# Optimization experiments

Hardware: AMD Instinct MI355X
Metric: run time of the kernel (lower is better)

Reference implementation:

```python
import jax, jax.numpy as jnp
import numpy as np

N_NODES = 50000
N_EDGES = 1600000
IN_C = 64
OUT_C = 64
N_CLASSES = 45


def setup_inputs() -> dict:
    key = jax.random.key(0)
    ks = jax.random.split(key, 12)

    def lin(k, i, o):
        return jax.random.normal(k, (i, o), jnp.float32) / np.float32(np.sqrt(i))

    return dict(
        x=jax.random.normal(ks[0], (N_NODES, IN_C), jnp.float32),
        edge_index=jax.random.randint(ks[1], (2, N_EDGES), 0, N_NODES, dtype=jnp.int32),
        W_z=lin(ks[2], IN_C, OUT_C), b_z=jnp.zeros((OUT_C,), jnp.float32),
        Wl_z=lin(ks[3], 2 * OUT_C, OUT_C), bl_z=jnp.zeros((OUT_C,), jnp.float32),
        W_r=lin(ks[4], IN_C, OUT_C), b_r=jnp.zeros((OUT_C,), jnp.float32),
        Wl_r=lin(ks[5], 2 * OUT_C, OUT_C), bl_r=jnp.zeros((OUT_C,), jnp.float32),
        W_h=lin(ks[6], IN_C, OUT_C), b_h=jnp.zeros((OUT_C,), jnp.float32),
        Wl_h=lin(ks[7], 2 * OUT_C, OUT_C), bl_h=jnp.zeros((OUT_C,), jnp.float32),
        W_out=lin(ks[8], OUT_C, N_CLASSES), b_out=jnp.zeros((N_CLASSES,), jnp.float32),
    )


def _gcn(x, W, b, src, dst, dinv):
    # GCNConv with improved self-loops (fill value 2.0):
    # out = D^{-1/2} (A + 2I) D^{-1/2} X W + b, with deg = in_degree + 2
    xw = x @ W                                   # [N, OUT_C]
    norm = dinv[src] * dinv[dst]                 # [E]
    agg = jax.ops.segment_sum(norm[:, None] * xw[src], dst, num_segments=N_NODES)
    agg = agg + (2.0 * dinv * dinv)[:, None] * xw  # self-loop contribution
    return agg + b


def reference(x, edge_index, W_z, b_z, Wl_z, bl_z, W_r, b_r, Wl_r, bl_r,
              W_h, b_h, Wl_h, bl_h, W_out, b_out):
    src, dst = edge_index[0], edge_index[1]
    deg = jax.ops.segment_sum(jnp.ones((N_EDGES,), jnp.float32), dst,
                              num_segments=N_NODES) + 2.0
    dinv = jax.lax.rsqrt(deg)

    # TGCN cell with H0 = 0 (no prior hidden state passed)
    H = jnp.zeros((N_NODES, OUT_C), x.dtype)
    Z = jax.nn.sigmoid(
        jnp.concatenate([_gcn(x, W_z, b_z, src, dst, dinv), H], axis=1) @ Wl_z + bl_z)
    R = jax.nn.sigmoid(
        jnp.concatenate([_gcn(x, W_r, b_r, src, dst, dinv), H], axis=1) @ Wl_r + bl_r)
    H_tilde = jnp.tanh(
        jnp.concatenate([_gcn(x, W_h, b_h, src, dst, dinv), H * R], axis=1) @ Wl_h + bl_h)
    H = Z * H + (1.0 - Z) * H_tilde

    # relu + linear readout to 45 classes
    return jax.nn.relu(H) @ W_out + b_out
```

## Files before the change

### kernel.cpp

```cpp
#include <hip/hip_runtime.h>

#define N_NODES 50000
#define N_EDGES 1600000
#define NB 782
#define NBB 256
#define CHUNK 6250
#define ZROW 50000
#define NTILES 3125

typedef unsigned short ushort_t;
typedef _Float16 v8h __attribute__((ext_vector_type(8)));
typedef float f32x4_t __attribute__((ext_vector_type(4)));

__device__ __forceinline__ int rlanei(int v, int l) {
  return __builtin_amdgcn_readlane(v, l);
}

__global__ void k_hist(const int* __restrict__ ei, int* __restrict__ cnt) {
  __shared__ int h[NB];
  int tid = threadIdx.x, blk = blockIdx.x;
  for (int i = tid; i < NB; i += 256) h[i] = 0;
  __syncthreads();
  int base = blk * CHUNK;
  for (int i = base + tid; i < base + CHUNK; i += 256)
    atomicAdd(&h[ei[N_EDGES + i] >> 6], 1);
  __syncthreads();
  for (int b = tid; b < NB; b += 256) cnt[b * NBB + blk] = h[b];
}

__global__ void k_scanA(const int* __restrict__ cnt, int* __restrict__ bsum) {
  __shared__ int sm[256];
  int t = threadIdx.x;
  sm[t] = cnt[blockIdx.x * 256 + t];
  __syncthreads();
  for (int off = 128; off > 0; off >>= 1) {
    if (t < off) sm[t] += sm[t + off];
    __syncthreads();
  }
  if (t == 0) bsum[blockIdx.x] = sm[0];
}

__global__ void k_scanB(const int* __restrict__ bsum, int* __restrict__ boff) {
  __shared__ int sm[1024];
  int t = threadIdx.x;
  int v = (t < NB) ? bsum[t] : 0;
  sm[t] = v;
  __syncthreads();
  for (int off = 1; off < 1024; off <<= 1) {
    int u = (t >= off) ? sm[t - off] : 0;
    __syncthreads();
    sm[t] += u;
    __syncthreads();
  }
  if (t < NB) boff[t] = sm[t] - v;
  if (t == 0) boff[NB] = N_EDGES;
}

__global__ void k_scanC(int* __restrict__ cnt, const int* __restrict__ boff) {
  __shared__ int sm[256];
  int t = threadIdx.x, j = blockIdx.x;
  int v = cnt[j * 256 + t];
  sm[t] = v;
  __syncthreads();
  for (int off = 1; off < 256; off <<= 1) {
    int u = (t >= off) ? sm[t - off] : 0;
    __syncthreads();
    sm[t] += u;
    __syncthreads();
  }
  cnt[j * 256 + t] = boff[j] + sm[t] - v;
}

__global__ void k_bin(const int* __restrict__ ei, const int* __restrict__ offs,
                      int* __restrict__ bins) {
  __shared__ int cur[NB];
  int tid = threadIdx.x, blk = blockIdx.x;
  for (int b = tid; b < NB; b += 256) cur[b] = offs[b * NBB + blk];
  __syncthreads();
  int base = blk * CHUNK;
  for (int i = base + tid; i < base + CHUNK; i += 256) {
    int s = ei[i];
    int d = ei[N_EDGES + i];
    int b = d >> 6;
    int p = atomicAdd(&cur[b], 1);
    bins[p] = s | ((d & 63) << 16);
  }
}

__global__ __launch_bounds__(256, 4) void k_sort(
    const int* __restrict__ bins, const int* __restrict__ boff,
    const float* __restrict__ x,
    ushort_t* __restrict__ srcp, int2* __restrict__ rowiv,
    float* __restrict__ dinv, _Float16* __restrict__ xp) {
  __shared__ int dg[64], lo[64], cur[64];
  __shared__ float sdin[64];
  __shared__ int Tsh;
  __shared__ ushort_t buf[8192];
  int tid = threadIdx.x, b = blockIdx.x;
  int start = boff[b], end = boff[b + 1];
  if (tid < 64) dg[tid] = 0;
  __syncthreads();
  for (int i = start + tid; i < end; i += 256)
    atomicAdd(&dg[bins[i] >> 16], 1);
  __syncthreads();
  int pdv = 0;
  if (tid < 64) { pdv = (dg[tid] + 7) & ~7; lo[tid] = pdv; }
  __syncthreads();
  for (int off = 1; off < 64; off <<= 1) {
    int u = 0;
    if (tid < 64 && tid >= off) u = lo[tid - off];
    __syncthreads();
    if (tid < 64) lo[tid] += u;
    __syncthreads();
  }
  int ex = 0;
  if (tid < 64) {
    ex = lo[tid] - pdv;
    cur[tid] = ex;
    if (tid == 63) Tsh = lo[63];
  }
  __syncthreads();
  int T = Tsh;
  int base = start + b * 512;
  for (int i = tid; i < T; i += 256) buf[i] = (ushort_t)ZROW;
  __syncthreads();
  for (int i = start + tid; i < end; i += 256) {
    int v = bins[i];
    int dl = v >> 16;
    int p = atomicAdd(&cur[dl], 1);
    buf[p] = (ushort_t)(v & 0xFFFF);
  }
  __syncthreads();
  for (int i = tid; i < T; i += 256) srcp[base + i] = buf[i];
  if (tid < 64) {
    int v = b * 64 + tid;
    if (v < N_NODES) {
      rowiv[v] = make_int2(base + ex, pdv);
      float dv = rsqrtf((float)dg[tid] + 2.0f);
      dinv[v] = dv;
      sdin[tid] = dv;
    } else {
      sdin[tid] = 0.f;
    }
  }
  __syncthreads();
  int nb64 = b * 4096;
  for (int idx = tid; idx < 4096; idx += 256) {
    int v = b * 64 + (idx >> 6);
    if (v < N_NODES) xp[nb64 + idx] = (_Float16)(sdin[idx >> 6] * x[nb64 + idx]);
  }
  if (b == 0 && tid < 64) xp[ZROW * 64 + tid] = (_Float16)0.f;
}

__global__ void k_compose(const float* __restrict__ Wz, const float* __restrict__ bz,
                          const float* __restrict__ Wlz, const float* __restrict__ blz,
                          const float* __restrict__ Wh, const float* __restrict__ bh,
                          const float* __restrict__ Wlh, const float* __restrict__ blh,
                          float2* __restrict__ M, float2* __restrict__ B2) {
  int t = blockIdx.x * 256 + threadIdx.x;
  if (t < 4096) {
    int i = t >> 6, c = t & 63;
    float mz = 0.f, mh = 0.f;
    for (int j = 0; j < 64; ++j) {
      mz = fmaf(Wz[i * 64 + j], Wlz[j * 64 + c], mz);
      mh = fmaf(Wh[i * 64 + j], Wlh[j * 64 + c], mh);
    }
    M[t] = make_float2(mz, mh);
  } else if (t < 4160) {
    int c = t - 4096;
    float vz = blz[c], vh = blh[c];
    for (int j = 0; j < 64; ++j) {
      vz = fmaf(bz[j], Wlz[j * 64 + c], vz);
      vh = fmaf(bh[j], Wlh[j * 64 + c], vh);
    }
    B2[c] = make_float2(vz, vh);
  }
}

__global__ void k_pack(const float2* __restrict__ M, const float* __restrict__ Wout,
                       _Float16* __restrict__ Bzh, _Float16* __restrict__ Bwo) {
  int t = blockIdx.x * 256 + threadIdx.x;
  if (t < 8192) {
    int frag = t >> 9, lane = (t >> 3) & 63, j = t & 7;
    int ntile = frag >> 1, ks = frag & 1;
    int n = ntile * 16 + (lane & 15);
    int k = ks * 32 + ((lane >> 4) << 3) + j;
    float v = (n < 64) ? M[k * 64 + n].x : M[k * 64 + (n - 64)].y;
    Bzh[t] = (_Float16)v;
  } else if (t < 11264) {
    int u = t - 8192;
    int frag = u >> 9, lane = (u >> 3) & 63, j = u & 7;
    int ntile = frag >> 1, ks = frag & 1;
    int n = ntile * 16 + (lane & 15);
    int k = ks * 32 + ((lane >> 4) << 3) + j;
    Bwo[u] = (_Float16)((n < 45) ? Wout[k * 45 + n] : 0.f);
  }
}

__global__ __launch_bounds__(256) void k_agg(
    const ushort_t* __restrict__ srcp, const int2* __restrict__ rowiv,
    const float* __restrict__ dinv, const _Float16* __restrict__ xp,
    _Float16* __restrict__ sxg) {
  int tid = threadIdx.x;
  int lane = tid & 63;
  int w = blockIdx.x * 4 + (tid >> 6);
  int nw = gridDim.x * 4;
  for (int v = w; v < N_NODES; v += nw) {
    int vu = __builtin_amdgcn_readfirstlane(v);
    int2 ri = rowiv[vu];
    int beg = ri.x, pd = ri.y;
    float a0 = 0.f, a1 = 0.f;
    for (int e = beg; e < beg + pd; e += 64) {
      int rem = beg + pd - e;
      int m = rem < 64 ? rem : 64;
      int sv = ZROW;
      if (lane < m) sv = srcp[e + lane];
      for (int j = 0; j < m; j += 8) {
        int s0 = rlanei(sv, j),     s1 = rlanei(sv, j + 1);
        int s2 = rlanei(sv, j + 2), s3 = rlanei(sv, j + 3);
        int s4 = rlanei(sv, j + 4), s5 = rlanei(sv, j + 5);
        int s6 = rlanei(sv, j + 6), s7 = rlanei(sv, j + 7);
        a0 += (float)xp[s0 * 64 + lane];
        a1 += (float)xp[s1 * 64 + lane];
        a0 += (float)xp[s2 * 64 + lane];
        a1 += (float)xp[s3 * 64 + lane];
        a0 += (float)xp[s4 * 64 + lane];
        a1 += (float)xp[s5 * 64 + lane];
        a0 += (float)xp[s6 * 64 + lane];
        a1 += (float)xp[s7 * 64 + lane];
      }
    }
    float dv = dinv[vu];
    float self = (float)xp[vu * 64 + lane];
    sxg[vu * 64 + lane] = (_Float16)(dv * (a0 + a1) + 2.f * dv * self);
  }
}

__global__ __launch_bounds__(256) void k_cell(
    const _Float16* __restrict__ sxg, const _Float16* __restrict__ Bzh,
    const _Float16* __restrict__ Bwo, const float2* __restrict__ B2,
    const float* __restrict__ bout, float* __restrict__ out) {
  __shared__ __align__(16) _Float16 tbuf[4][16][72];
  int tid = threadIdx.x;
  int lane = tid & 63, wv = tid >> 6;
  int l15 = lane & 15, quad = lane >> 4;
  int tile = blockIdx.x * 4 + wv;
  if (tile >= NTILES) return;

  v8h bz[8][2], bw[3][2];
  #pragma unroll
  for (int t = 0; t < 8; ++t)
    #pragma unroll
    for (int ks = 0; ks < 2; ++ks)
      bz[t][ks] = *(const v8h*)(Bzh + (((t * 2 + ks) * 64 + lane) << 3));
  #pragma unroll
  for (int t = 0; t < 3; ++t)
    #pragma unroll
    for (int ks = 0; ks < 2; ++ks)
      bw[t][ks] = *(const v8h*)(Bwo + (((t * 2 + ks) * 64 + lane) << 3));
  float zb[4], hb[4], ob[3];
  #pragma unroll
  for (int t = 0; t < 4; ++t) {
    float2 bb = B2[t * 16 + l15];
    zb[t] = bb.x; hb[t] = bb.y;
  }
  #pragma unroll
  for (int t = 0; t < 3; ++t) {
    int c = t * 16 + l15;
    ob[t] = (c < 45) ? bout[c] : 0.f;
  }

  const _Float16* ar = sxg + (tile * 16 + l15) * 64 + quad * 8;
  v8h a0 = *(const v8h*)ar;
  v8h a1 = *(const v8h*)(ar + 32);

  f32x4_t accz[8];
  #pragma unroll
  for (int t = 0; t < 8; ++t) {
    f32x4_t c4 = {0.f, 0.f, 0.f, 0.f};
    c4 = __builtin_amdgcn_mfma_f32_16x16x32_f16(a0, bz[t][0], c4, 0, 0, 0);
    c4 = __builtin_amdgcn_mfma_f32_16x16x32_f16(a1, bz[t][1], c4, 0, 0, 0);
    accz[t] = c4;
  }

  #pragma unroll
  for (int t = 0; t < 4; ++t) {
    #pragma unroll
    for (int r = 0; r < 4; ++r) {
      float zv = accz[t][r] + zb[t];
      float hv = accz[t + 4][r] + hb[t];
      float Z = 1.f / (1.f + __expf(-zv));
      float tt = fminf(15.f, fmaxf(-15.f, hv));
      float e2 = __expf(-2.f * tt);
      float Th = (1.f - e2) / (1.f + e2);
      tbuf[wv][quad * 4 + r][t * 16 + l15] = (_Float16)fmaxf((1.f - Z) * Th, 0.f);
    }
  }
  __asm__ volatile("s_waitcnt lgkmcnt(0)" ::: "memory");

  v8h p0 = *(const v8h*)&tbuf[wv][l15][quad * 8];
  v8h p1 = *(const v8h*)&tbuf[wv][l15][32 + quad * 8];

  #pragma unroll
  for (int t = 0; t < 3; ++t) {
    f32x4_t o4 = {0.f, 0.f, 0.f, 0.f};
    o4 = __builtin_amdgcn_mfma_f32_16x16x32_f16(p0, bw[t][0], o4, 0, 0, 0);
    o4 = __builtin_amdgcn_mfma_f32_16x16x32_f16(p1, bw[t][1], o4, 0, 0, 0);
    int c = t * 16 + l15;
    if (c < 45) {
      #pragma unroll
      for (int r = 0; r < 4; ++r)
        out[(tile * 16 + quad * 4 + r) * 45 + c] = o4[r] + ob[t];
    }
  }
}

extern "C" void kernel_launch(void* const* d_in, const int* in_sizes, int n_in,
                              void* d_out, int out_size, void* d_ws, size_t ws_size,
                              hipStream_t stream) {
  const float* x    = (const float*)d_in[0];
  const int*   ei   = (const int*)d_in[1];
  const float* Wz   = (const float*)d_in[2];
  const float* bz   = (const float*)d_in[3];
  const float* Wlz  = (const float*)d_in[4];
  const float* blz  = (const float*)d_in[5];
  const float* Wh   = (const float*)d_in[10];
  const float* bh   = (const float*)d_in[11];
  const float* Wlh  = (const float*)d_in[12];
  const float* blh  = (const float*)d_in[13];
  const float* Wout = (const float*)d_in[14];
  const float* bout = (const float*)d_in[15];
  float* out = (float*)d_out;

  char* w = (char*)d_ws;
  int*      cnt   = (int*)(w + 0);
  int*      bins  = (int*)(w + 800768);
  _Float16* sxg   = (_Float16*)(w + 0);
  ushort_t* srcp  = (ushort_t*)(w + 12800000);
  int2*     rowiv = (int2*)(w + 16801024);
  float*    dinv  = (float*)(w + 17201024);
  int*      bsum  = (int*)(w + 17401024);
  int*      boff  = (int*)(w + 17404160);
  float2*   M     = (float2*)(w + 17407360);
  float2*   B2    = (float2*)(w + 17440128);
  _Float16* Bzh   = (_Float16*)(w + 17440768);
  _Float16* Bwo   = (_Float16*)(w + 17457152);
  _Float16* xp    = (_Float16*)(w + 17463296);

  k_hist <<<NBB, 256, 0, stream>>>(ei, cnt);
  k_scanA<<<NB, 256, 0, stream>>>(cnt, bsum);
  k_scanB<<<1, 1024, 0, stream>>>(bsum, boff);
  k_scanC<<<NB, 256, 0, stream>>>(cnt, boff);
  k_bin  <<<NBB, 256, 0, stream>>>(ei, cnt, bins);
  k_sort <<<NB, 256, 0, stream>>>(bins, boff, x, srcp, rowiv, dinv, xp);
  k_compose<<<17, 256, 0, stream>>>(Wz, bz, Wlz, blz, Wh, bh, Wlh, blh, M, B2);
  k_pack <<<44, 256, 0, stream>>>(M, Wout, Bzh, Bwo);
  k_agg  <<<2048, 256, 0, stream>>>(srcp, rowiv, dinv, xp, sxg);
  k_cell <<<NB, 256, 0, stream>>>(sxg, Bzh, Bwo, B2, bout, out);
}
```

Measured before the change: 191.8 us.

## Fuse CSR build into one cooperative kernel with grid syncs; merge weight prep

Replaces the histogram, three scan kernels, binning and per-bucket sort kernels with a single cooperative kernel that uses grid.sync between phases. Each block bins its edge chunk locally in shared memory and records per-bucket local offsets, then gathers its bucket's edges from every chunk. The weight composition and packing kernels are merged into one kernel that writes MFMA-layout fragments directly. The aim is to cut kernel launch count and inter-kernel gaps, at the cost of grid-wide barriers, a scattered gather of many tiny segments per block, and a requirement that all 782 blocks be co-resident.

```diff
diff --git a/kernel.cpp b/kernel.cpp
--- a/kernel.cpp
+++ b/kernel.cpp
@@ -1,10 +1,12 @@
 #include <hip/hip_runtime.h>
+#include <hip/hip_cooperative_groups.h>
+namespace cg = cooperative_groups;
 
 #define N_NODES 50000
 #define N_EDGES 1600000
 #define NB 782
-#define NBB 256
-#define CHUNK 6250
+#define NBK 782
+#define CH 2048
 #define ZROW 50000
 #define NTILES 3125
 
@@ -16,92 +18,116 @@
   return __builtin_amdgcn_readlane(v, l);
 }
 
-__global__ void k_hist(const int* __restrict__ ei, int* __restrict__ cnt) {
+__global__ __launch_bounds__(256, 4) void k_build(
+    const int* __restrict__ ei, int* __restrict__ cnt, int* __restrict__ bsum,
+    ushort_t* __restrict__ loc, int* __restrict__ bins,
+    const float* __restrict__ x, ushort_t* __restrict__ srcp,
+    int2* __restrict__ rowiv, float* __restrict__ dinv,
+    _Float16* __restrict__ xp) {
   __shared__ int h[NB];
+  __shared__ int hB[NB];
+  __shared__ int ebuf[3072];
+  __shared__ ushort_t buf[3584];
+  __shared__ int scanTmp[256];
+  __shared__ int dg[64], lo[64], cur64[64];
+  __shared__ float sdin[64];
+  __shared__ int misc[4];
+  cg::grid_group grid = cg::this_grid();
   int tid = threadIdx.x, blk = blockIdx.x;
+  int e0 = blk * CH;
+  int e1 = min(e0 + CH, N_EDGES);
+  int clen = e1 - e0;
+
   for (int i = tid; i < NB; i += 256) h[i] = 0;
   __syncthreads();
-  int base = blk * CHUNK;
-  for (int i = base + tid; i < base + CHUNK; i += 256)
+  for (int i = e0 + tid; i < e1; i += 256)
     atomicAdd(&h[ei[N_EDGES + i] >> 6], 1);
   __syncthreads();
-  for (int b = tid; b < NB; b += 256) cnt[b * NBB + blk] = h[b];
-}
-
-__global__ void k_scanA(const int* __restrict__ cnt, int* __restrict__ bsum) {
-  __shared__ int sm[256];
-  int t = threadIdx.x;
-  sm[t] = cnt[blockIdx.x * 256 + t];
-  __syncthreads();
-  for (int off = 128; off > 0; off >>= 1) {
-    if (t < off) sm[t] += sm[t + off];
-    __syncthreads();
-  }
-  if (t == 0) bsum[blockIdx.x] = sm[0];
-}
-
-__global__ void k_scanB(const int* __restrict__ bsum, int* __restrict__ boff) {
-  __shared__ int sm[1024];
-  int t = threadIdx.x;
-  int v = (t < NB) ? bsum[t] : 0;
-  sm[t] = v;
-  __syncthreads();
-  for (int off = 1; off < 1024; off <<= 1) {
-    int u = (t >= off) ? sm[t - off] : 0;
-    __syncthreads();
-    sm[t] += u;
-    __syncthreads();
-  }
-  if (t < NB) boff[t] = sm[t] - v;
-  if (t == 0) boff[NB] = N_EDGES;
-}
-
-__global__ void k_scanC(int* __restrict__ cnt, const int* __restrict__ boff) {
-  __shared__ int sm[256];
-  int t = threadIdx.x, j = blockIdx.x;
-  int v = cnt[j * 256 + t];
-  sm[t] = v;
-  __syncthreads();
-  for (int off = 1; off < 256; off <<= 1) {
-    int u = (t >= off) ? sm[t - off] : 0;
-    __syncthreads();
-    sm[t] += u;
-    __syncthreads();
-  }
-  cnt[j * 256 + t] = boff[j] + sm[t] - v;
-}
-
-__global__ void k_bin(const int* __restrict__ ei, const int* __restrict__ offs,
-                      int* __restrict__ bins) {
-  __shared__ int cur[NB];
-  int tid = threadIdx.x, blk = blockIdx.x;
-  for (int b = tid; b < NB; b += 256) cur[b] = offs[b * NBB + blk];
-  __syncthreads();
-  int base = blk * CHUNK;
-  for (int i = base + tid; i < base + CHUNK; i += 256) {
-    int s = ei[i];
-    int d = ei[N_EDGES + i];
-    int b = d >> 6;
-    int p = atomicAdd(&cur[b], 1);
-    bins[p] = s | ((d & 63) << 16);
-  }
-}
-
-__global__ __launch_bounds__(256, 4) void k_sort(
-    const int* __restrict__ bins, const int* __restrict__ boff,
-    const float* __restrict__ x,
-    ushort_t* __restrict__ srcp, int2* __restrict__ rowiv,
-    float* __restrict__ dinv, _Float16* __restrict__ xp) {
-  __shared__ int dg[64], lo[64], cur[64];
-  __shared__ float sdin[64];
-  __shared__ int Tsh;
-  __shared__ ushort_t buf[8192];
-  int tid = threadIdx.x, b = blockIdx.x;
-  int start = boff[b], end = boff[b + 1];
+  for (int b = tid; b < NB; b += 256) cnt[blk * NB + b] = h[b];
+  grid.sync();
+
+  {
+    int part = 0;
+    for (int i = tid; i < NBK; i += 256) part += cnt[i * NB + blk];
+    scanTmp[tid] = part;
+    __syncthreads();
+    for (int off = 128; off > 0; off >>= 1) {
+      if (tid < off) scanTmp[tid] += scanTmp[tid + off];
+      __syncthreads();
+    }
+    if (tid == 0) bsum[blk] = scanTmp[0];
+    __syncthreads();
+  }
+
+  {
+    int vals[4]; int ts = 0;
+    int base4 = tid * 4;
+    #pragma unroll
+    for (int r = 0; r < 4; ++r) {
+      int idx = base4 + r;
+      int v = (idx < NB) ? h[idx] : 0;
+      vals[r] = v; ts += v;
+    }
+    scanTmp[tid] = ts;
+    __syncthreads();
+    for (int off = 1; off < 256; off <<= 1) {
+      int u = (tid >= off) ? scanTmp[tid - off] : 0;
+      __syncthreads();
+      scanTmp[tid] += u;
+      __syncthreads();
+    }
+    int ex = scanTmp[tid] - ts;
+    #pragma unroll
+    for (int r = 0; r < 4; ++r) {
+      int idx = base4 + r;
+      if (idx < NB) {
+        hB[idx] = ex;
+        loc[blk * (NB + 1) + idx] = (ushort_t)ex;
+      }
+      ex += vals[r];
+    }
+    if (tid == 0) loc[blk * (NB + 1) + NB] = (ushort_t)clen;
+    __syncthreads();
+    for (int i = e0 + tid; i < e1; i += 256) {
+      int s = ei[i];
+      int d = ei[N_EDGES + i];
+      int p = atomicAdd(&hB[d >> 6], 1);
+      ebuf[p] = s | ((d & 63) << 16);
+    }
+    __syncthreads();
+    for (int i = tid; i < clen; i += 256) bins[e0 + i] = ebuf[i];
+  }
+  grid.sync();
+
+  int b = blk;
+  {
+    int part = 0;
+    for (int j = tid; j < b; j += 256) part += bsum[j];
+    scanTmp[tid] = part;
+    __syncthreads();
+    for (int off = 128; off > 0; off >>= 1) {
+      if (tid < off) scanTmp[tid] += scanTmp[tid + off];
+      __syncthreads();
+    }
+    if (tid == 0) { misc[1] = scanTmp[0]; misc[0] = 0; }
+    __syncthreads();
+  }
+  int boffb = misc[1];
+  for (int j = tid; j < NBK; j += 256) {
+    int l0 = loc[j * (NB + 1) + b];
+    int l1 = loc[j * (NB + 1) + b + 1];
+    int len = l1 - l0;
+    if (len > 0) {
+      int pos = atomicAdd(&misc[0], len);
+      for (int k2 = 0; k2 < len; ++k2)
+        ebuf[pos + k2] = bins[j * CH + l0 + k2];
+    }
+  }
+  __syncthreads();
+  int nEd = misc[0];
   if (tid < 64) dg[tid] = 0;
   __syncthreads();
-  for (int i = start + tid; i < end; i += 256)
-    atomicAdd(&dg[bins[i] >> 16], 1);
+  for (int i = tid; i < nEd; i += 256) atomicAdd(&dg[ebuf[i] >> 16], 1);
   __syncthreads();
   int pdv = 0;
   if (tid < 64) { pdv = (dg[tid] + 7) & ~7; lo[tid] = pdv; }
@@ -113,29 +139,28 @@
     if (tid < 64) lo[tid] += u;
     __syncthreads();
   }
-  int ex = 0;
+  int ex2 = 0;
   if (tid < 64) {
-    ex = lo[tid] - pdv;
-    cur[tid] = ex;
-    if (tid == 63) Tsh = lo[63];
-  }
-  __syncthreads();
-  int T = Tsh;
-  int base = start + b * 512;
+    ex2 = lo[tid] - pdv;
+    cur64[tid] = ex2;
+    if (tid == 63) misc[2] = lo[63];
+  }
+  __syncthreads();
+  int T = misc[2];
+  int sbase = boffb + b * 512;
   for (int i = tid; i < T; i += 256) buf[i] = (ushort_t)ZROW;
   __syncthreads();
-  for (int i = start + tid; i < end; i += 256) {
-    int v = bins[i];
-    int dl = v >> 16;
-    int p = atomicAdd(&cur[dl], 1);
+  for (int i = tid; i < nEd; i += 256) {
+    int v = ebuf[i];
+    int p = atomicAdd(&cur64[v >> 16], 1);
     buf[p] = (ushort_t)(v & 0xFFFF);
   }
   __syncthreads();
-  for (int i = tid; i < T; i += 256) srcp[base + i] = buf[i];
+  for (int i = tid; i < T; i += 256) srcp[sbase + i] = buf[i];
   if (tid < 64) {
     int v = b * 64 + tid;
     if (v < N_NODES) {
-      rowiv[v] = make_int2(base + ex, pdv);
+      rowiv[v] = make_int2(sbase + ex2, pdv);
       float dv = rsqrtf((float)dg[tid] + 2.0f);
       dinv[v] = dv;
       sdin[tid] = dv;
@@ -152,48 +177,43 @@
   if (b == 0 && tid < 64) xp[ZROW * 64 + tid] = (_Float16)0.f;
 }
 
-__global__ void k_compose(const float* __restrict__ Wz, const float* __restrict__ bz,
-                          const float* __restrict__ Wlz, const float* __restrict__ blz,
-                          const float* __restrict__ Wh, const float* __restrict__ bh,
-                          const float* __restrict__ Wlh, const float* __restrict__ blh,
-                          float2* __restrict__ M, float2* __restrict__ B2) {
+__global__ __launch_bounds__(256) void k_wprep(
+    const float* __restrict__ Wz, const float* __restrict__ bz,
+    const float* __restrict__ Wlz, const float* __restrict__ blz,
+    const float* __restrict__ Wh, const float* __restrict__ bh,
+    const float* __restrict__ Wlh, const float* __restrict__ blh,
+    const float* __restrict__ Wout,
+    float2* __restrict__ B2, _Float16* __restrict__ Bzh,
+    _Float16* __restrict__ Bwo) {
   int t = blockIdx.x * 256 + threadIdx.x;
-  if (t < 4096) {
-    int i = t >> 6, c = t & 63;
-    float mz = 0.f, mh = 0.f;
-    for (int j = 0; j < 64; ++j) {
-      mz = fmaf(Wz[i * 64 + j], Wlz[j * 64 + c], mz);
-      mh = fmaf(Wh[i * 64 + j], Wlh[j * 64 + c], mh);
-    }
-    M[t] = make_float2(mz, mh);
-  } else if (t < 4160) {
-    int c = t - 4096;
-    float vz = blz[c], vh = blh[c];
-    for (int j = 0; j < 64; ++j) {
-      vz = fmaf(bz[j], Wlz[j * 64 + c], vz);
-      vh = fmaf(bh[j], Wlh[j * 64 + c], vh);
-    }
-    B2[c] = make_float2(vz, vh);
-  }
-}
-
-__global__ void k_pack(const float2* __restrict__ M, const float* __restrict__ Wout,
-                       _Float16* __restrict__ Bzh, _Float16* __restrict__ Bwo) {
-  int t = blockIdx.x * 256 + threadIdx.x;
-  if (t < 8192) {
-    int frag = t >> 9, lane = (t >> 3) & 63, j = t & 7;
-    int ntile = frag >> 1, ks = frag & 1;
+  {
+    int lane = (t >> 3) & 63, j = t & 7;
+    int ntile = t >> 10, ks = (t >> 9) & 1;
     int n = ntile * 16 + (lane & 15);
     int k = ks * 32 + ((lane >> 4) << 3) + j;
-    float v = (n < 64) ? M[k * 64 + n].x : M[k * 64 + (n - 64)].y;
-    Bzh[t] = (_Float16)v;
-  } else if (t < 11264) {
-    int u = t - 8192;
-    int frag = u >> 9, lane = (u >> 3) & 63, j = u & 7;
-    int ntile = frag >> 1, ks = frag & 1;
+    float acc = 0.f;
+    if (n < 64) {
+      for (int q = 0; q < 64; ++q) acc = fmaf(Wz[k * 64 + q], Wlz[q * 64 + n], acc);
+    } else {
+      int n2 = n - 64;
+      for (int q = 0; q < 64; ++q) acc = fmaf(Wh[k * 64 + q], Wlh[q * 64 + n2], acc);
+    }
+    Bzh[t] = (_Float16)acc;
+  }
+  if (t < 3072) {
+    int lane = (t >> 3) & 63, j = t & 7;
+    int ntile = t >> 10, ks = (t >> 9) & 1;
     int n = ntile * 16 + (lane & 15);
     int k = ks * 32 + ((lane >> 4) << 3) + j;
-    Bwo[u] = (_Float16)((n < 45) ? Wout[k * 45 + n] : 0.f);
+    Bwo[t] = (_Float16)((n < 45) ? Wout[k * 45 + n] : 0.f);
+  }
+  if (t < 64) {
+    float vz = blz[t], vh = blh[t];
+    for (int q = 0; q < 64; ++q) {
+      vz = fmaf(bz[q], Wlz[q * 64 + t], vz);
+      vh = fmaf(bh[q], Wlh[q * 64 + t], vh);
+    }
+    B2[t] = make_float2(vz, vh);
   }
 }
 
@@ -247,17 +267,17 @@
   int tile = blockIdx.x * 4 + wv;
   if (tile >= NTILES) return;
 
-  v8h bz[8][2], bw[3][2];
+  v8h bzf[8][2], bwf[3][2];
   #pragma unroll
   for (int t = 0; t < 8; ++t)
     #pragma unroll
     for (int ks = 0; ks < 2; ++ks)
-      bz[t][ks] = *(const v8h*)(Bzh + (((t * 2 + ks) * 64 + lane) << 3));
+      bzf[t][ks] = *(const v8h*)(Bzh + (((t * 2 + ks) * 64 + lane) << 3));
   #pragma unroll
   for (int t = 0; t < 3; ++t)
     #pragma unroll
     for (int ks = 0; ks < 2; ++ks)
-      bw[t][ks] = *(const v8h*)(Bwo + (((t * 2 + ks) * 64 + lane) << 3));
+      bwf[t][ks] = *(const v8h*)(Bwo + (((t * 2 + ks) * 64 + lane) << 3));
   float zb[4], hb[4], ob[3];
   #pragma unroll
   for (int t = 0; t < 4; ++t) {
@@ -278,8 +298,8 @@
   #pragma unroll
   for (int t = 0; t < 8; ++t) {
     f32x4_t c4 = {0.f, 0.f, 0.f, 0.f};
-    c4 = __builtin_amdgcn_mfma_f32_16x16x32_f16(a0, bz[t][0], c4, 0, 0, 0);
-    c4 = __builtin_amdgcn_mfma_f32_16x16x32_f16(a1, bz[t][1], c4, 0, 0, 0);
+    c4 = __builtin_amdgcn_mfma_f32_16x16x32_f16(a0, bzf[t][0], c4, 0, 0, 0);
+    c4 = __builtin_amdgcn_mfma_f32_16x16x32_f16(a1, bzf[t][1], c4, 0, 0, 0);
     accz[t] = c4;
   }
 
@@ -304,8 +324,8 @@
   #pragma unroll
   for (int t = 0; t < 3; ++t) {
     f32x4_t o4 = {0.f, 0.f, 0.f, 0.f};
-    o4 = __builtin_amdgcn_mfma_f32_16x16x32_f16(p0, bw[t][0], o4, 0, 0, 0);
-    o4 = __builtin_amdgcn_mfma_f32_16x16x32_f16(p1, bw[t][1], o4, 0, 0, 0);
+    o4 = __builtin_amdgcn_mfma_f32_16x16x32_f16(p0, bwf[t][0], o4, 0, 0, 0);
+    o4 = __builtin_amdgcn_mfma_f32_16x16x32_f16(p1, bwf[t][1], o4, 0, 0, 0);
     int c = t * 16 + l15;
     if (c < 45) {
       #pragma unroll
@@ -334,27 +354,27 @@
 
   char* w = (char*)d_ws;
   int*      cnt   = (int*)(w + 0);
-  int*      bins  = (int*)(w + 800768);
+  int*      bins  = (int*)(w + 2446096);
+  ushort_t* loc   = (ushort_t*)(w + 8846096);
+  int*      bsum  = (int*)(w + 10070720);
   _Float16* sxg   = (_Float16*)(w + 0);
-  ushort_t* srcp  = (ushort_t*)(w + 12800000);
-  int2*     rowiv = (int2*)(w + 16801024);
-  float*    dinv  = (float*)(w + 17201024);
-  int*      bsum  = (int*)(w + 17401024);
-  int*      boff  = (int*)(w + 17404160);
-  float2*   M     = (float2*)(w + 17407360);
-  float2*   B2    = (float2*)(w + 17440128);
-  _Float16* Bzh   = (_Float16*)(w + 17440768);
-  _Float16* Bwo   = (_Float16*)(w + 17457152);
-  _Float16* xp    = (_Float16*)(w + 17463296);
-
-  k_hist <<<NBB, 256, 0, stream>>>(ei, cnt);
-  k_scanA<<<NB, 256, 0, stream>>>(cnt, bsum);
-  k_scanB<<<1, 1024, 0, stream>>>(bsum, boff);
-  k_scanC<<<NB, 256, 0, stream>>>(cnt, boff);
-  k_bin  <<<NBB, 256, 0, stream>>>(ei, cnt, bins);
-  k_sort <<<NB, 256, 0, stream>>>(bins, boff, x, srcp, rowiv, dinv, xp);
-  k_compose<<<17, 256, 0, stream>>>(Wz, bz, Wlz, blz, Wh, bh, Wlh, blh, M, B2);
-  k_pack <<<44, 256, 0, stream>>>(M, Wout, Bzh, Bwo);
-  k_agg  <<<2048, 256, 0, stream>>>(srcp, rowiv, dinv, xp, sxg);
-  k_cell <<<NB, 256, 0, stream>>>(sxg, Bzh, Bwo, B2, bout, out);
-}
+  ushort_t* srcp  = (ushort_t*)(w + 10073856);
+  int2*     rowiv = (int2*)(w + 14074624);
+  float*    dinv  = (float*)(w + 14474624);
+  float2*   B2    = (float2*)(w + 14674624);
+  _Float16* Bzh   = (_Float16*)(w + 14675136);
+  _Float16* Bwo   = (_Float16*)(w + 14691520);
+  _Float16* xp    = (_Float16*)(w + 14697664);
+
+  k_wprep<<<32, 256, 0, stream>>>(Wz, bz, Wlz, blz, Wh, bh, Wlh, blh, Wout,
+                                  B2, Bzh, Bwo);
+  {
+    void* args[] = {(void*)&ei, (void*)&cnt, (void*)&bsum, (void*)&loc,
+                    (void*)&bins, (void*)&x, (void*)&srcp, (void*)&rowiv,
+                    (void*)&dinv, (void*)&xp};
+    hipLaunchCooperativeKernel((const void*)k_build, dim3(NBK), dim3(256),
+                               args, 0, stream);
+  }
+  k_agg <<<2048, 256, 0, stream>>>(srcp, rowiv, dinv, xp, sxg);
+  k_cell<<<NB, 256, 0, stream>>>(sxg, Bzh, Bwo, B2, bout, out);
+}
```

Result: slower. 362.5 us (+89.0%).

## Vectorize agg gathers by splitting wave into 4 edge groups; merge weight-prep kernels

Applied to the files above, without the earlier changes.

The aggregation kernel now splits each wave into four 16-lane groups. Each group gathers a different edge's row using 8-byte half4 loads, with two edges per group per step, and the partial sums are reduced across groups with xor shuffles. Previously each edge took one 2-byte-per-lane load across all 64 lanes. Histogram and binning kernels read edge indices as int2 pairs, and the compose and pack weight kernels are fused into one launch that moves ahead of the graph pipeline. This cuts load instruction count and launch overhead, at the cost of extra cross-lane shuffles and fp32 reductions per node.

```diff
diff --git a/kernel.cpp b/kernel.cpp
--- a/kernel.cpp
+++ b/kernel.cpp
@@ -10,6 +10,7 @@
 
 typedef unsigned short ushort_t;
 typedef _Float16 v8h __attribute__((ext_vector_type(8)));
+typedef _Float16 v4h __attribute__((ext_vector_type(4)));
 typedef float f32x4_t __attribute__((ext_vector_type(4)));
 
 __device__ __forceinline__ int rlanei(int v, int l) {
@@ -21,9 +22,12 @@
   int tid = threadIdx.x, blk = blockIdx.x;
   for (int i = tid; i < NB; i += 256) h[i] = 0;
   __syncthreads();
-  int base = blk * CHUNK;
-  for (int i = base + tid; i < base + CHUNK; i += 256)
-    atomicAdd(&h[ei[N_EDGES + i] >> 6], 1);
+  const int2* d2 = (const int2*)(ei + N_EDGES + blk * CHUNK);
+  for (int i = tid; i < CHUNK / 2; i += 256) {
+    int2 d = d2[i];
+    atomicAdd(&h[d.x >> 6], 1);
+    atomicAdd(&h[d.y >> 6], 1);
+  }
   __syncthreads();
   for (int b = tid; b < NB; b += 256) cnt[b * NBB + blk] = h[b];
 }
@@ -77,13 +81,15 @@
   int tid = threadIdx.x, blk = blockIdx.x;
   for (int b = tid; b < NB; b += 256) cur[b] = offs[b * NBB + blk];
   __syncthreads();
-  int base = blk * CHUNK;
-  for (int i = base + tid; i < base + CHUNK; i += 256) {
-    int s = ei[i];
-    int d = ei[N_EDGES + i];
-    int b = d >> 6;
-    int p = atomicAdd(&cur[b], 1);
-    bins[p] = s | ((d & 63) << 16);
+  const int2* s2 = (const int2*)(ei + blk * CHUNK);
+  const int2* d2 = (const int2*)(ei + N_EDGES + blk * CHUNK);
+  for (int i = tid; i < CHUNK / 2; i += 256) {
+    int2 s = s2[i];
+    int2 d = d2[i];
+    int p0 = atomicAdd(&cur[d.x >> 6], 1);
+    bins[p0] = s.x | ((d.x & 63) << 16);
+    int p1 = atomicAdd(&cur[d.y >> 6], 1);
+    bins[p1] = s.y | ((d.y & 63) << 16);
   }
 }
 
@@ -152,48 +158,43 @@
   if (b == 0 && tid < 64) xp[ZROW * 64 + tid] = (_Float16)0.f;
 }
 
-__global__ void k_compose(const float* __restrict__ Wz, const float* __restrict__ bz,
-                          const float* __restrict__ Wlz, const float* __restrict__ blz,
-                          const float* __restrict__ Wh, const float* __restrict__ bh,
-                          const float* __restrict__ Wlh, const float* __restrict__ blh,
-                          float2* __restrict__ M, float2* __restrict__ B2) {
+__global__ __launch_bounds__(256) void k_wprep(
+    const float* __restrict__ Wz, const float* __restrict__ bz,
+    const float* __restrict__ Wlz, const float* __restrict__ blz,
+    const float* __restrict__ Wh, const float* __restrict__ bh,
+    const float* __restrict__ Wlh, const float* __restrict__ blh,
+    const float* __restrict__ Wout,
+    float2* __restrict__ B2, _Float16* __restrict__ Bzh,
+    _Float16* __restrict__ Bwo) {
   int t = blockIdx.x * 256 + threadIdx.x;
-  if (t < 4096) {
-    int i = t >> 6, c = t & 63;
-    float mz = 0.f, mh = 0.f;
-    for (int j = 0; j < 64; ++j) {
-      mz = fmaf(Wz[i * 64 + j], Wlz[j * 64 + c], mz);
-      mh = fmaf(Wh[i * 64 + j], Wlh[j * 64 + c], mh);
-    }
-    M[t] = make_float2(mz, mh);
-  } else if (t < 4160) {
-    int c = t - 4096;
-    float vz = blz[c], vh = blh[c];
-    for (int j = 0; j < 64; ++j) {
-      vz = fmaf(bz[j], Wlz[j * 64 + c], vz);
-      vh = fmaf(bh[j], Wlh[j * 64 + c], vh);
-    }
-    B2[c] = make_float2(vz, vh);
-  }
-}
-
-__global__ void k_pack(const float2* __restrict__ M, const float* __restrict__ Wout,
-                       _Float16* __restrict__ Bzh, _Float16* __restrict__ Bwo) {
-  int t = blockIdx.x * 256 + threadIdx.x;
-  if (t < 8192) {
-    int frag = t >> 9, lane = (t >> 3) & 63, j = t & 7;
-    int ntile = frag >> 1, ks = frag & 1;
+  {
+    int lane = (t >> 3) & 63, j = t & 7;
+    int ntile = t >> 10, ks = (t >> 9) & 1;
     int n = ntile * 16 + (lane & 15);
     int k = ks * 32 + ((lane >> 4) << 3) + j;
-    float v = (n < 64) ? M[k * 64 + n].x : M[k * 64 + (n - 64)].y;
-    Bzh[t] = (_Float16)v;
-  } else if (t < 11264) {
-    int u = t - 8192;
-    int frag = u >> 9, lane = (u >> 3) & 63, j = u & 7;
-    int ntile = frag >> 1, ks = frag & 1;
+    float acc = 0.f;
+    if (n < 64) {
+      for (int q = 0; q < 64; ++q) acc = fmaf(Wz[k * 64 + q], Wlz[q * 64 + n], acc);
+    } else {
+      int n2 = n - 64;
+      for (int q = 0; q < 64; ++q) acc = fmaf(Wh[k * 64 + q], Wlh[q * 64 + n2], acc);
+    }
+    Bzh[t] = (_Float16)acc;
+  }
+  if (t < 3072) {
+    int lane = (t >> 3) & 63, j = t & 7;
+    int ntile = t >> 10, ks = (t >> 9) & 1;
     int n = ntile * 16 + (lane & 15);
     int k = ks * 32 + ((lane >> 4) << 3) + j;
-    Bwo[u] = (_Float16)((n < 45) ? Wout[k * 45 + n] : 0.f);
+    Bwo[t] = (_Float16)((n < 45) ? Wout[k * 45 + n] : 0.f);
+  }
+  if (t < 64) {
+    float vz = blz[t], vh = blh[t];
+    for (int q = 0; q < 64; ++q) {
+      vz = fmaf(bz[q], Wlz[q * 64 + t], vz);
+      vh = fmaf(bh[q], Wlh[q * 64 + t], vh);
+    }
+    B2[t] = make_float2(vz, vh);
   }
 }
 
@@ -203,36 +204,47 @@
     _Float16* __restrict__ sxg) {
   int tid = threadIdx.x;
   int lane = tid & 63;
+  int grp = lane >> 4;
+  int sub = lane & 15;
+  int chOff = sub << 2;
   int w = blockIdx.x * 4 + (tid >> 6);
   int nw = gridDim.x * 4;
   for (int v = w; v < N_NODES; v += nw) {
     int vu = __builtin_amdgcn_readfirstlane(v);
     int2 ri = rowiv[vu];
     int beg = ri.x, pd = ri.y;
-    float a0 = 0.f, a1 = 0.f;
+    float aA0 = 0.f, aA1 = 0.f, aA2 = 0.f, aA3 = 0.f;
+    float aB0 = 0.f, aB1 = 0.f, aB2 = 0.f, aB3 = 0.f;
     for (int e = beg; e < beg + pd; e += 64) {
       int rem = beg + pd - e;
       int m = rem < 64 ? rem : 64;
-      int sv = ZROW;
-      if (lane < m) sv = srcp[e + lane];
-      for (int j = 0; j < m; j += 8) {
-        int s0 = rlanei(sv, j),     s1 = rlanei(sv, j + 1);
-        int s2 = rlanei(sv, j + 2), s3 = rlanei(sv, j + 3);
-        int s4 = rlanei(sv, j + 4), s5 = rlanei(sv, j + 5);
-        int s6 = rlanei(sv, j + 6), s7 = rlanei(sv, j + 7);
-        a0 += (float)xp[s0 * 64 + lane];
-        a1 += (float)xp[s1 * 64 + lane];
-        a0 += (float)xp[s2 * 64 + lane];
-        a1 += (float)xp[s3 * 64 + lane];
-        a0 += (float)xp[s4 * 64 + lane];
-        a1 += (float)xp[s5 * 64 + lane];
-        a0 += (float)xp[s6 * 64 + lane];
-        a1 += (float)xp[s7 * 64 + lane];
+      int sv = (lane < m) ? (int)srcp[e + lane] : ZROW;
+      for (int t = 0; t < m; t += 8) {
+        int sA = __builtin_amdgcn_ds_bpermute((t + grp) << 2, sv);
+        int sB = __builtin_amdgcn_ds_bpermute((t + 4 + grp) << 2, sv);
+        v4h rA = *(const v4h*)(xp + (sA << 6) + chOff);
+        v4h rB = *(const v4h*)(xp + (sB << 6) + chOff);
+        aA0 += (float)rA[0]; aA1 += (float)rA[1];
+        aA2 += (float)rA[2]; aA3 += (float)rA[3];
+        aB0 += (float)rB[0]; aB1 += (float)rB[1];
+        aB2 += (float)rB[2]; aB3 += (float)rB[3];
       }
     }
-    float dv = dinv[vu];
-    float self = (float)xp[vu * 64 + lane];
-    sxg[vu * 64 + lane] = (_Float16)(dv * (a0 + a1) + 2.f * dv * self);
+    float a0 = aA0 + aB0, a1 = aA1 + aB1, a2 = aA2 + aB2, a3 = aA3 + aB3;
+    a0 += __shfl_xor(a0, 16); a1 += __shfl_xor(a1, 16);
+    a2 += __shfl_xor(a2, 16); a3 += __shfl_xor(a3, 16);
+    a0 += __shfl_xor(a0, 32); a1 += __shfl_xor(a1, 32);
+    a2 += __shfl_xor(a2, 32); a3 += __shfl_xor(a3, 32);
+    if (lane < 16) {
+      float dv = dinv[vu];
+      v4h self = *(const v4h*)(xp + (vu << 6) + chOff);
+      v4h o;
+      o[0] = (_Float16)(dv * a0 + 2.f * dv * (float)self[0]);
+      o[1] = (_Float16)(dv * a1 + 2.f * dv * (float)self[1]);
+      o[2] = (_Float16)(dv * a2 + 2.f * dv * (float)self[2]);
+      o[3] = (_Float16)(dv * a3 + 2.f * dv * (float)self[3]);
+      *(v4h*)(sxg + (vu << 6) + chOff) = o;
+    }
   }
 }
 
@@ -247,17 +259,17 @@
   int tile = blockIdx.x * 4 + wv;
   if (tile >= NTILES) return;
 
-  v8h bz[8][2], bw[3][2];
+  v8h bzf[8][2], bwf[3][2];
   #pragma unroll
   for (int t = 0; t < 8; ++t)
     #pragma unroll
     for (int ks = 0; ks < 2; ++ks)
-      bz[t][ks] = *(const v8h*)(Bzh + (((t * 2 + ks) * 64 + lane) << 3));
+      bzf[t][ks] = *(const v8h*)(Bzh + (((t * 2 + ks) * 64 + lane) << 3));
   #pragma unroll
   for (int t = 0; t < 3; ++t)
     #pragma unroll
     for (int ks = 0; ks < 2; ++ks)
-      bw[t][ks] = *(const v8h*)(Bwo + (((t * 2 + ks) * 64 + lane) << 3));
+      bwf[t][ks] = *(const v8h*)(Bwo + (((t * 2 + ks) * 64 + lane) << 3));
   float zb[4], hb[4], ob[3];
   #pragma unroll
   for (int t = 0; t < 4; ++t) {
@@ -278,8 +290,8 @@
   #pragma unroll
   for (int t = 0; t < 8; ++t) {
     f32x4_t c4 = {0.f, 0.f, 0.f, 0.f};
-    c4 = __builtin_amdgcn_mfma_f32_16x16x32_f16(a0, bz[t][0], c4, 0, 0, 0);
-    c4 = __builtin_amdgcn_mfma_f32_16x16x32_f16(a1, bz[t][1], c4, 0, 0, 0);
+    c4 = __builtin_amdgcn_mfma_f32_16x16x32_f16(a0, bzf[t][0], c4, 0, 0, 0);
+    c4 = __builtin_amdgcn_mfma_f32_16x16x32_f16(a1, bzf[t][1], c4, 0, 0, 0);
     accz[t] = c4;
   }
 
@@ -304,8 +316,8 @@
   #pragma unroll
   for (int t = 0; t < 3; ++t) {
     f32x4_t o4 = {0.f, 0.f, 0.f, 0.f};
-    o4 = __builtin_amdgcn_mfma_f32_16x16x32_f16(p0, bw[t][0], o4, 0, 0, 0);
-    o4 = __builtin_amdgcn_mfma_f32_16x16x32_f16(p1, bw[t][1], o4, 0, 0, 0);
+    o4 = __builtin_amdgcn_mfma_f32_16x16x32_f16(p0, bwf[t][0], o4, 0, 0, 0);
+    o4 = __builtin_amdgcn_mfma_f32_16x16x32_f16(p1, bwf[t][1], o4, 0, 0, 0);
     int c = t * 16 + l15;
     if (c < 45) {
       #pragma unroll
@@ -341,20 +353,19 @@
   float*    dinv  = (float*)(w + 17201024);
   int*      bsum  = (int*)(w + 17401024);
   int*      boff  = (int*)(w + 17404160);
-  float2*   M     = (float2*)(w + 17407360);
   float2*   B2    = (float2*)(w + 17440128);
   _Float16* Bzh   = (_Float16*)(w + 17440768);
   _Float16* Bwo   = (_Float16*)(w + 17457152);
   _Float16* xp    = (_Float16*)(w + 17463296);
 
+  k_wprep<<<32, 256, 0, stream>>>(Wz, bz, Wlz, blz, Wh, bh, Wlh, blh, Wout,
+                                  B2, Bzh, Bwo);
   k_hist <<<NBB, 256, 0, stream>>>(ei, cnt);
   k_scanA<<<NB, 256, 0, stream>>>(cnt, bsum);
   k_scanB<<<1, 1024, 0, stream>>>(bsum, boff);
   k_scanC<<<NB, 256, 0, stream>>>(cnt, boff);
   k_bin  <<<NBB, 256, 0, stream>>>(ei, cnt, bins);
   k_sort <<<NB, 256, 0, stream>>>(bins, boff, x, srcp, rowiv, dinv, xp);
-  k_compose<<<17, 256, 0, stream>>>(Wz, bz, Wlz, blz, Wh, bh, Wlh, blh, M, B2);
-  k_pack <<<44, 256, 0, stream>>>(M, Wout, Bzh, Bwo);
   k_agg  <<<2048, 256, 0, stream>>>(srcp, rowiv, dinv, xp, sxg);
   k_cell <<<NB, 256, 0, stream>>>(sxg, Bzh, Bwo, B2, bout, out);
 }
```

Measured after the change: 179.0 us. -6.6%, faster.
